# Kernel tuning notes

Measured on AMD Instinct MI355X. Metric: run time of the kernel, lower is better.

Reference implementation:

```python
import jax, jax.numpy as jnp
import numpy as np

NUM_HEADS = 12
THETA = 10000.0

def apply_rope(x, pos, theta):
    # x: [B, H, S, d_k]; pos: [S]
    d_k = x.shape[-1]
    inv_freq = theta ** (-jnp.arange(0, d_k, 2, dtype=jnp.float32) / d_k)  # [d_k/2]
    ang = pos[:, None].astype(jnp.float32) * inv_freq[None, :]             # [S, d_k/2]
    cos, sin = jnp.cos(ang), jnp.sin(ang)
    x1, x2 = x[..., ::2], x[..., 1::2]
    out_even = x1 * cos - x2 * sin
    out_odd = x1 * sin + x2 * cos
    # interleave back to [..., d_k]
    return jnp.stack([out_even, out_odd], axis=-1).reshape(x.shape)

def setup_inputs() -> dict:
    key = jax.random.key(0)
    ks = jax.random.split(key, 5)
    B, S, D = 1, 4096, 768
    x = jax.random.normal(ks[0], (B, S, D), dtype=jnp.float32)
    scale = 0.02
    Wq = jax.random.normal(ks[1], (D, D), dtype=jnp.float32) * scale
    Wk = jax.random.normal(ks[2], (D, D), dtype=jnp.float32) * scale
    Wv = jax.random.normal(ks[3], (D, D), dtype=jnp.float32) * scale
    Wo = jax.random.normal(ks[4], (D, D), dtype=jnp.float32) * scale
    return {"x": x, "Wq": Wq, "Wk": Wk, "Wv": Wv, "Wo": Wo}

def reference(x, Wq, Wk, Wv, Wo):
    B, S, D = x.shape
    H = NUM_HEADS
    d_k = D // H
    # projections (torch Linear: y = x @ W.T, no bias)
    Q = x @ Wq.T
    K = x @ Wk.T
    V = x @ Wv.T
    # [B, S, H*d_k] -> [B, H, S, d_k]
    def split_heads(t):
        return t.reshape(B, S, H, d_k).transpose(0, 2, 1, 3)
    Q, K, V = split_heads(Q), split_heads(K), split_heads(V)
    pos = jnp.arange(S)
    Q = apply_rope(Q, pos, THETA)
    K = apply_rope(K, pos, THETA)
    scores = jnp.einsum('bhnd,bhmd->bhnm', Q, K) * (d_k ** -0.5)  # [B,H,S,S]
    causal = jnp.tril(jnp.ones((S, S), dtype=bool))
    scores = jnp.where(causal, scores, -jnp.inf)
    attn = jax.nn.softmax(scores, axis=-1)
    out = jnp.einsum('bhnm,bhmd->bhnd', attn, V)  # [B,H,S,d_k]
    out = out.transpose(0, 2, 1, 3).reshape(B, S, D)
    return out @ Wo.T
```

## Files before the change

### kernel.cpp

```cpp
#include <hip/hip_runtime.h>
#include <hip/hip_bf16.h>
#include <cstdint>

typedef __bf16 bf16x8 __attribute__((ext_vector_type(8)));
typedef float f32x4 __attribute__((ext_vector_type(4)));
typedef float f32x16 __attribute__((ext_vector_type(16)));

static constexpr int S = 4096;
static constexpr int D = 768;
static constexpr int DK = 64;

__device__ __forceinline__ unsigned short f2bf(float f) {
  unsigned u = __float_as_uint(f);
  u = (u + 0x7fffu + ((u >> 16) & 1u)) >> 16;
  return (unsigned short)u;
}

__global__ __launch_bounds__(256) void cvt5_kernel(
    const float* __restrict__ x, const float* __restrict__ wq,
    const float* __restrict__ wk, const float* __restrict__ wv,
    const float* __restrict__ wo,
    unsigned short* __restrict__ xb, unsigned short* __restrict__ wqb,
    unsigned short* __restrict__ wkb, unsigned short* __restrict__ wvb,
    unsigned short* __restrict__ wob, float2* __restrict__ tab) {
  int i = blockIdx.x * blockDim.x + threadIdx.x;
  constexpr int NX4 = (S * D) / 4;
  constexpr int NW4 = (D * D) / 4;
  constexpr int NC = NX4 + 4 * NW4;
  if (i < NC) {
    const float* src;
    unsigned short* dst;
    int off;
    if (i < NX4)               { src = x;  dst = xb;  off = i; }
    else if (i < NX4 + NW4)    { src = wq; dst = wqb; off = i - NX4; }
    else if (i < NX4 + 2*NW4)  { src = wk; dst = wkb; off = i - NX4 - NW4; }
    else if (i < NX4 + 3*NW4)  { src = wv; dst = wvb; off = i - NX4 - 2*NW4; }
    else                       { src = wo; dst = wob; off = i - NX4 - 3*NW4; }
    float4 v = reinterpret_cast<const float4*>(src)[off];
    ushort4 o;
    o.x = f2bf(v.x); o.y = f2bf(v.y); o.z = f2bf(v.z); o.w = f2bf(v.w);
    reinterpret_cast<ushort4*>(dst)[off] = o;
  } else {
    int idx = i - NC;
    if (idx < S * 32) {
      int s = idx >> 5, ii = idx & 31;
      float freq = expf(-(float)(2 * ii) * (9.210340371976184f / 64.0f));
      float si, c;
      sincosf((float)s * freq, &si, &c);
      tab[idx] = make_float2(c, si);
    }
  }
}

__global__ __launch_bounds__(512) void qkv_gemm_kernel(
    const unsigned short* __restrict__ xb,
    const unsigned short* __restrict__ Wall,
    const float2* __restrict__ tab,
    unsigned short* __restrict__ Qh,
    unsigned short* __restrict__ Kf,
    unsigned short* __restrict__ Vf) {
  __shared__ alignas(16) unsigned short At[2][128 * 64];
  __shared__ alignas(16) unsigned short Bt[2][128 * 64];

  const int t = threadIdx.x;
  const int lane = t & 63;
  const int lr = lane & 15;
  const int hi = lane >> 4;
  const int wave = t >> 6;
  const int wr = wave >> 1, wc = wave & 1;
  const int row0 = blockIdx.x * 128;
  const int n0 = blockIdx.y * 128;
  const int sx = lr & 7;

  f32x4 acc[2][4] = {};

  auto stage = [&](int buf, int k0) {
#pragma unroll
    for (int j = 0; j < 2; ++j) {
      const int ci = wave * 128 + j * 64 + lane;
      const int row = ci >> 3;
      const int c16 = ci & 7;
      const int csrc = (c16 ^ (row & 7)) * 8;
      __builtin_amdgcn_global_load_lds(
          (const __attribute__((address_space(1))) void*)(
              xb + (size_t)(row0 + row) * 768 + k0 + csrc),
          (__attribute__((address_space(3))) void*)(&At[buf][row * 64 + c16 * 8]),
          16, 0, 0);
      __builtin_amdgcn_global_load_lds(
          (const __attribute__((address_space(1))) void*)(
              Wall + (size_t)(n0 + row) * 768 + k0 + csrc),
          (__attribute__((address_space(3))) void*)(&Bt[buf][row * 64 + c16 * 8]),
          16, 0, 0);
    }
  };

  stage(0, 0);
  __syncthreads();

#pragma unroll
  for (int ts = 0; ts < 12; ++ts) {
    const int cur = ts & 1;
    if (ts + 1 < 12) stage(cur ^ 1, (ts + 1) * 64);
#pragma unroll
    for (int kk = 0; kk < 2; ++kk) {
      const int csw = ((kk * 4 + hi) ^ sx) * 8;
      bf16x8 a[2], b[4];
#pragma unroll
      for (int rf = 0; rf < 2; ++rf)
        a[rf] = *reinterpret_cast<const bf16x8*>(
            &At[cur][(wr * 32 + rf * 16 + lr) * 64 + csw]);
#pragma unroll
      for (int nf = 0; nf < 4; ++nf)
        b[nf] = *reinterpret_cast<const bf16x8*>(
            &Bt[cur][(wc * 64 + nf * 16 + lr) * 64 + csw]);
#pragma unroll
      for (int rf = 0; rf < 2; ++rf)
#pragma unroll
        for (int nf = 0; nf < 4; ++nf)
          acc[rf][nf] = __builtin_amdgcn_mfma_f32_16x16x32_bf16(a[rf], b[nf], acc[rf][nf], 0, 0, 0);
    }
    __syncthreads();
  }

  const int z = n0 / 768;

  if (z < 2) {
#pragma unroll
    for (int nf = 0; nf < 4; ++nf) {
      const int c = n0 - z * 768 + wc * 64 + nf * 16 + lr;
      const int hh = c >> 6;
      const int dk = c & 63;
      const int ii = dk >> 1;
#pragma unroll
      for (int rf = 0; rf < 2; ++rf) {
        const int jrow = row0 + wr * 32 + rf * 16 + hi * 4;
#pragma unroll
        for (int j = 0; j < 4; ++j) {
          float v = acc[rf][nf][j];
          const int s = jrow + j;
          float pv = __shfl_xor(v, 1);
          float2 cs = tab[(size_t)s * 32 + ii];
          v = (dk & 1) ? (pv * cs.y + v * cs.x) : (v * cs.x - pv * cs.y);
          if (z == 0) {
            Qh[((size_t)hh * S + s) * DK + dk] = f2bf(v * 0.18033688f);
          } else {
            const size_t koff = ((size_t)hh * 128 + (s >> 5)) * 2048 +
                                (size_t)(dk >> 4) * 512 + ((dk >> 3) & 1) * 256 +
                                (s & 31) * 8 + (dk & 7);
            Kf[koff] = f2bf(v);
          }
        }
      }
    }
  } else {
#pragma unroll
    for (int nf = 0; nf < 4; ++nf) {
      const int c = n0 - 1536 + wc * 64 + nf * 16 + lr;
      const int hh = c >> 6;
      const int dv = c & 63;
#pragma unroll
      for (int rf = 0; rf < 2; ++rf) {
        const int jrow = row0 + wr * 32 + rf * 16 + hi * 4;
#pragma unroll
        for (int j = 0; j < 4; ++j) {
          const int s = jrow + j;
          const size_t voff = ((size_t)hh * 256 + (s >> 4)) * 1024 +
                              (size_t)(dv >> 5) * 512 + (dv & 31) * 16 +
                              ((s >> 3) & 1) * 8 + (s & 7);
          Vf[voff] = f2bf(acc[rf][nf][j]);
        }
      }
    }
  }
}

__global__ __launch_bounds__(256) void attn_kernel(
    const unsigned short* __restrict__ Qh,
    const unsigned short* __restrict__ Kf,
    const unsigned short* __restrict__ Vf,
    unsigned short* __restrict__ AO) {
  const int c = blockIdx.x;
  const int sslot = blockIdx.y;
  const int m3 = 3 * (c >> 1);
  const int g = sslot / 3, r = sslot - 3 * g;
  int h, qt;
  if ((c & 1) == 0) {
    if (r == 0)      { h = m3;     qt = 127 - 2 * g; }
    else if (r == 1) { h = m3 + 1; qt = 127 - 2 * g; }
    else             { h = m3;     qt = 126 - 2 * g; }
  } else {
    if (r == 0)      { h = m3 + 2; qt = 127 - 2 * g; }
    else if (r == 1) { h = m3 + 2; qt = 126 - 2 * g; }
    else             { h = m3 + 1; qt = 126 - 2 * g; }
  }

  const int wave = threadIdx.x >> 6;
  const int lane = threadIdx.x & 63;
  const int lq = lane & 31;
  const int hi2 = lane >> 5;
  const int q0w = qt * 32;
  const int qg = q0w + lq;

  const unsigned short* Qp = Qh + ((size_t)h * S + qg) * DK + hi2 * 8;
  const unsigned short* Kfp = Kf + (size_t)h * (S * DK) + hi2 * 256 + lq * 8;
  const unsigned short* Vfp = Vf + (size_t)h * (S * DK) + lq * 16 + hi2 * 8;

  bf16x8 qf[4];
#pragma unroll
  for (int ks = 0; ks < 4; ++ks)
    qf[ks] = *reinterpret_cast<const bf16x8*>(Qp + ks * 16);

  f32x16 acc0 = {}, acc1 = {};
  float lsum[4] = {0.f, 0.f, 0.f, 0.f};

  const int kvmax = ((q0w + 31) >> 6) << 6;
  const int kvfirst = 64 * wave;

  bf16x8 ka[2][4];
  if (kvfirst <= kvmax) {
    const unsigned short* K0 = Kfp + ((size_t)(kvfirst >> 5)) * 2048;
#pragma unroll
    for (int tt = 0; tt < 2; ++tt)
#pragma unroll
      for (int ks = 0; ks < 4; ++ks)
        ka[tt][ks] = *reinterpret_cast<const bf16x8*>(K0 + (size_t)tt * 2048 + ks * 512);
  }

  for (int kv0 = kvfirst; kv0 <= kvmax; kv0 += 256) {
    bf16x8 vb[2][4];
#pragma unroll
    for (int dvh = 0; dvh < 2; ++dvh)
#pragma unroll
      for (int ks = 0; ks < 4; ++ks)
        vb[dvh][ks] = *reinterpret_cast<const bf16x8*>(
            Vfp + ((size_t)(kv0 >> 4) + ks) * 1024 + dvh * 512);

    f32x16 s0 = {}, s1 = {};
#pragma unroll
    for (int ks = 0; ks < 4; ++ks) {
      s0 = __builtin_amdgcn_mfma_f32_32x32x16_bf16(ka[0][ks], qf[ks], s0, 0, 0, 0);
      s1 = __builtin_amdgcn_mfma_f32_32x32x16_bf16(ka[1][ks], qf[ks], s1, 0, 0, 0);
    }

    if ((kv0 + 256) <= kvmax) {
      const unsigned short* Kn = Kfp + ((size_t)((kv0 + 256) >> 5)) * 2048;
#pragma unroll
      for (int tt = 0; tt < 2; ++tt)
#pragma unroll
        for (int ks = 0; ks < 4; ++ks)
          ka[tt][ks] = *reinterpret_cast<const bf16x8*>(Kn + (size_t)tt * 2048 + ks * 512);
    }

    if ((kv0 + 63) > q0w) {
#pragma unroll
      for (int rr = 0; rr < 16; ++rr) {
        const int kvr = kv0 + (rr & 3) + 8 * (rr >> 2) + 4 * hi2;
        if (kvr > qg) s0[rr] = -1e30f;
        if (kvr + 32 > qg) s1[rr] = -1e30f;
      }
    }

#pragma unroll
    for (int rr = 0; rr < 16; ++rr) {
      float e0, e1;
      asm("v_exp_f32 %0, %1" : "=v"(e0) : "v"(s0[rr]));
      asm("v_exp_f32 %0, %1" : "=v"(e1) : "v"(s1[rr]));
      s0[rr] = e0;
      s1[rr] = e1;
      lsum[rr & 3] += e0 + e1;
    }

    bf16x8 pa[4];
#pragma unroll
    for (int ks = 0; ks < 4; ++ks) {
      const int a4 = 8 * (ks & 1);
      unsigned X01, X23, Y01, Y23;
      if (ks < 2) {
        asm("v_cvt_pk_bf16_f32 %0, %1, %2" : "=v"(X01) : "v"(s0[a4 + 0]), "v"(s0[a4 + 1]));
        asm("v_cvt_pk_bf16_f32 %0, %1, %2" : "=v"(X23) : "v"(s0[a4 + 2]), "v"(s0[a4 + 3]));
        asm("v_cvt_pk_bf16_f32 %0, %1, %2" : "=v"(Y01) : "v"(s0[a4 + 4]), "v"(s0[a4 + 5]));
        asm("v_cvt_pk_bf16_f32 %0, %1, %2" : "=v"(Y23) : "v"(s0[a4 + 6]), "v"(s0[a4 + 7]));
      } else {
        asm("v_cvt_pk_bf16_f32 %0, %1, %2" : "=v"(X01) : "v"(s1[a4 + 0]), "v"(s1[a4 + 1]));
        asm("v_cvt_pk_bf16_f32 %0, %1, %2" : "=v"(X23) : "v"(s1[a4 + 2]), "v"(s1[a4 + 3]));
        asm("v_cvt_pk_bf16_f32 %0, %1, %2" : "=v"(Y01) : "v"(s1[a4 + 4]), "v"(s1[a4 + 5]));
        asm("v_cvt_pk_bf16_f32 %0, %1, %2" : "=v"(Y23) : "v"(s1[a4 + 6]), "v"(s1[a4 + 7]));
      }
      asm volatile("v_permlane32_swap_b32 %0, %1" : "+v"(X01), "+v"(Y01));
      asm volatile("v_permlane32_swap_b32 %0, %1" : "+v"(X23), "+v"(Y23));
      union { unsigned u[4]; bf16x8 v; } P;
      P.u[0] = X01; P.u[1] = X23; P.u[2] = Y01; P.u[3] = Y23;
      pa[ks] = P.v;
    }

#pragma unroll
    for (int ks = 0; ks < 4; ++ks) {
      acc0 = __builtin_amdgcn_mfma_f32_32x32x16_bf16(pa[ks], vb[0][ks], acc0, 0, 0, 0);
      acc1 = __builtin_amdgcn_mfma_f32_32x32x16_bf16(pa[ks], vb[1][ks], acc1, 0, 0, 0);
    }
  }

  const float lw = (lsum[0] + lsum[1]) + (lsum[2] + lsum[3]);
  const float l_ = lw + __shfl_xor(lw, 32);

  __shared__ float llds[4][32];
  __shared__ float obuf[4][64][17];

  if (hi2 == 0) llds[wave][lq] = l_;

#pragma unroll
  for (int rr = 0; rr < 16; ++rr) obuf[wave][lane][rr] = acc0[rr];
  __syncthreads();

  const float Ltot = llds[0][lq] + llds[1][lq] + llds[2][lq] + llds[3][lq];
  const float linv = 1.0f / Ltot;

  float v0[4];
#pragma unroll
  for (int rr = 0; rr < 4; ++rr) {
    const int rq = wave * 4 + rr;
    v0[rr] = obuf[0][lane][rq] + obuf[1][lane][rq] + obuf[2][lane][rq] + obuf[3][lane][rq];
  }
  __syncthreads();

#pragma unroll
  for (int rr = 0; rr < 16; ++rr) obuf[wave][lane][rr] = acc1[rr];
  __syncthreads();

#pragma unroll
  for (int rr = 0; rr < 4; ++rr) {
    const int rq = wave * 4 + rr;
    const float v1 = obuf[0][lane][rq] + obuf[1][lane][rq] + obuf[2][lane][rq] + obuf[3][lane][rq];
    const int row = (rq & 3) + 8 * (rq >> 2) + 4 * hi2;
    const float li = __shfl(linv, row);
    const size_t s = q0w + row;
    AO[s * D + h * DK + lq]      = f2bf(v0[rr] * li);
    AO[s * D + h * DK + 32 + lq] = f2bf(v1 * li);
  }
}

__global__ __launch_bounds__(256) void oproj_kernel(
    const unsigned short* __restrict__ AO,
    const unsigned short* __restrict__ Wob,
    float* __restrict__ out) {
  __shared__ alignas(16) unsigned short At[2][128 * 64];
  __shared__ alignas(16) unsigned short Bt[2][128 * 64];

  const int t = threadIdx.x;
  const int lane = t & 63;
  const int lr = lane & 15;
  const int hi = lane >> 4;
  const int wave = t >> 6;
  const int wr = wave >> 1, wc = wave & 1;
  const int row0 = blockIdx.x * 128;
  const int n0 = blockIdx.y * 128;

  const int trow = t >> 3;
  const int tc8  = (t & 7) * 8;
  const int tsw8 = (((t & 7) ^ (trow & 7)) * 8);
  const int sx = lr & 7;

  f32x4 acc[4][4] = {};

  auto stage = [&](int buf, int k0) {
#pragma unroll
    for (int i = 0; i < 4; ++i) {
      __builtin_amdgcn_global_load_lds(
          (const __attribute__((address_space(1))) void*)(
              AO + (size_t)(row0 + trow + 32 * i) * 768 + k0 + tsw8),
          (__attribute__((address_space(3))) void*)(&At[buf][(trow + 32 * i) * 64 + tc8]),
          16, 0, 0);
      __builtin_amdgcn_global_load_lds(
          (const __attribute__((address_space(1))) void*)(
              Wob + (size_t)(n0 + trow + 32 * i) * 768 + k0 + tsw8),
          (__attribute__((address_space(3))) void*)(&Bt[buf][(trow + 32 * i) * 64 + tc8]),
          16, 0, 0);
    }
  };

  stage(0, 0);
  __syncthreads();

#pragma unroll
  for (int ts = 0; ts < 12; ++ts) {
    const int cur = ts & 1;
    if (ts + 1 < 12) stage(cur ^ 1, (ts + 1) * 64);
#pragma unroll
    for (int kk = 0; kk < 2; ++kk) {
      const int csw = ((kk * 4 + hi) ^ sx) * 8;
      bf16x8 a[4], b[4];
#pragma unroll
      for (int rf = 0; rf < 4; ++rf)
        a[rf] = *reinterpret_cast<const bf16x8*>(
            &At[cur][(wr * 64 + rf * 16 + lr) * 64 + csw]);
#pragma unroll
      for (int nf = 0; nf < 4; ++nf)
        b[nf] = *reinterpret_cast<const bf16x8*>(
            &Bt[cur][(wc * 64 + nf * 16 + lr) * 64 + csw]);
#pragma unroll
      for (int rf = 0; rf < 4; ++rf)
#pragma unroll
        for (int nf = 0; nf < 4; ++nf)
          acc[rf][nf] = __builtin_amdgcn_mfma_f32_16x16x32_bf16(a[rf], b[nf], acc[rf][nf], 0, 0, 0);
    }
    __syncthreads();
  }

#pragma unroll
  for (int rf = 0; rf < 4; ++rf) {
    const int jrow = row0 + wr * 64 + rf * 16 + hi * 4;
#pragma unroll
    for (int nf = 0; nf < 4; ++nf) {
      const int cn = n0 + wc * 64 + nf * 16 + lr;
#pragma unroll
      for (int j = 0; j < 4; ++j)
        out[(size_t)(jrow + j) * D + cn] = acc[rf][nf][j];
    }
  }
}

extern "C" void kernel_launch(void* const* d_in, const int* in_sizes, int n_in,
                              void* d_out, int out_size, void* d_ws, size_t ws_size,
                              hipStream_t stream) {
  const float* x  = (const float*)d_in[0];
  const float* Wq = (const float*)d_in[1];
  const float* Wk = (const float*)d_in[2];
  const float* Wv = (const float*)d_in[3];
  const float* Wo = (const float*)d_in[4];
  float* out = (float*)d_out;

  char* ws = (char*)d_ws;
  unsigned short* xb  = (unsigned short*)(ws + 0);
  unsigned short* Wqb = (unsigned short*)(ws + 6291456);
  unsigned short* Wkb = (unsigned short*)(ws + 7471104);
  unsigned short* Wvb = (unsigned short*)(ws + 8650752);
  unsigned short* Wob = (unsigned short*)(ws + 9830400);
  unsigned short* Qh  = (unsigned short*)(ws + 11010048);
  unsigned short* Kf  = (unsigned short*)(ws + 17301504);
  unsigned short* Vf  = (unsigned short*)(ws + 23592960);
  unsigned short* AO  = (unsigned short*)(ws + 29884416);
  float2* tab = (float2*)(ws + 29884416);

  cvt5_kernel<<<5888, 256, 0, stream>>>(x, Wq, Wk, Wv, Wo, xb, Wqb, Wkb, Wvb, Wob, tab);
  qkv_gemm_kernel<<<dim3(32, 18), 512, 0, stream>>>(xb, Wqb, tab, Qh, Kf, Vf);
  attn_kernel<<<dim3(8, 192), 256, 0, stream>>>(Qh, Kf, Vf, AO);
  oproj_kernel<<<dim3(32, 6), 256, 0, stream>>>(AO, Wob, out);
}
```

Baseline: 102.1 us.

## Halve oproj row tile to 64 and split attention row-sum accumulators

The output-projection GEMM now uses 64x128 tiles instead of 128x128, doubling the grid from 192 to 384 blocks so more of the GPU's compute units are busy. Staging loads are reorganised to fit the smaller A tile. In the attention kernel, the softmax denominator now uses 16 independent partial sums instead of 4, shortening the add dependency chains, with a tree reduction at the end. The smaller tile lowers per-block reuse of the Wo tile and adds some extra registers.

```diff
diff --git a/kernel.cpp b/kernel.cpp
--- a/kernel.cpp
+++ b/kernel.cpp
@@ -211,7 +211,9 @@
     qf[ks] = *reinterpret_cast<const bf16x8*>(Qp + ks * 16);
 
   f32x16 acc0 = {}, acc1 = {};
-  float lsum[4] = {0.f, 0.f, 0.f, 0.f};
+  float lsum[16];
+#pragma unroll
+  for (int r2 = 0; r2 < 16; ++r2) lsum[r2] = 0.f;
 
   const int kvmax = ((q0w + 31) >> 6) << 6;
   const int kvfirst = 64 * wave;
@@ -267,7 +269,7 @@
       asm("v_exp_f32 %0, %1" : "=v"(e1) : "v"(s1[rr]));
       s0[rr] = e0;
       s1[rr] = e1;
-      lsum[rr & 3] += e0 + e1;
+      lsum[rr] += e0 + e1;
     }
 
     bf16x8 pa[4];
@@ -300,8 +302,12 @@
     }
   }
 
-  const float lw = (lsum[0] + lsum[1]) + (lsum[2] + lsum[3]);
-  const float l_ = lw + __shfl_xor(lw, 32);
+#pragma unroll
+  for (int off = 8; off > 0; off >>= 1)
+#pragma unroll
+    for (int rr = 0; rr < 8; ++rr)
+      if (rr < off) lsum[rr] += lsum[rr + off];
+  const float l_ = lsum[0] + __shfl_xor(lsum[0], 32);
 
   __shared__ float llds[4][32];
   __shared__ float obuf[4][64][17];
@@ -343,7 +349,7 @@
     const unsigned short* __restrict__ AO,
     const unsigned short* __restrict__ Wob,
     float* __restrict__ out) {
-  __shared__ alignas(16) unsigned short At[2][128 * 64];
+  __shared__ alignas(16) unsigned short At[2][64 * 64];
   __shared__ alignas(16) unsigned short Bt[2][128 * 64];
 
   const int t = threadIdx.x;
@@ -352,28 +358,35 @@
   const int hi = lane >> 4;
   const int wave = t >> 6;
   const int wr = wave >> 1, wc = wave & 1;
-  const int row0 = blockIdx.x * 128;
+  const int row0 = blockIdx.x * 64;
   const int n0 = blockIdx.y * 128;
-
-  const int trow = t >> 3;
-  const int tc8  = (t & 7) * 8;
-  const int tsw8 = (((t & 7) ^ (trow & 7)) * 8);
   const int sx = lr & 7;
 
-  f32x4 acc[4][4] = {};
+  f32x4 acc[2][4] = {};
 
   auto stage = [&](int buf, int k0) {
 #pragma unroll
-    for (int i = 0; i < 4; ++i) {
+    for (int p = 0; p < 2; ++p) {
+      const int ci = p * 256 + t;
+      const int row = ci >> 3;
+      const int c16 = ci & 7;
+      const int csrc = (c16 ^ (row & 7)) * 8;
       __builtin_amdgcn_global_load_lds(
           (const __attribute__((address_space(1))) void*)(
-              AO + (size_t)(row0 + trow + 32 * i) * 768 + k0 + tsw8),
-          (__attribute__((address_space(3))) void*)(&At[buf][(trow + 32 * i) * 64 + tc8]),
+              AO + (size_t)(row0 + row) * 768 + k0 + csrc),
+          (__attribute__((address_space(3))) void*)(&At[buf][row * 64 + c16 * 8]),
           16, 0, 0);
+    }
+#pragma unroll
+    for (int p = 0; p < 4; ++p) {
+      const int ci = p * 256 + t;
+      const int row = ci >> 3;
+      const int c16 = ci & 7;
+      const int csrc = (c16 ^ (row & 7)) * 8;
       __builtin_amdgcn_global_load_lds(
           (const __attribute__((address_space(1))) void*)(
-              Wob + (size_t)(n0 + trow + 32 * i) * 768 + k0 + tsw8),
-          (__attribute__((address_space(3))) void*)(&Bt[buf][(trow + 32 * i) * 64 + tc8]),
+              Wob + (size_t)(n0 + row) * 768 + k0 + csrc),
+          (__attribute__((address_space(3))) void*)(&Bt[buf][row * 64 + c16 * 8]),
           16, 0, 0);
     }
   };
@@ -388,17 +401,17 @@
 #pragma unroll
     for (int kk = 0; kk < 2; ++kk) {
       const int csw = ((kk * 4 + hi) ^ sx) * 8;
-      bf16x8 a[4], b[4];
-#pragma unroll
-      for (int rf = 0; rf < 4; ++rf)
+      bf16x8 a[2], b[4];
+#pragma unroll
+      for (int rf = 0; rf < 2; ++rf)
         a[rf] = *reinterpret_cast<const bf16x8*>(
-            &At[cur][(wr * 64 + rf * 16 + lr) * 64 + csw]);
+            &At[cur][(wr * 32 + rf * 16 + lr) * 64 + csw]);
 #pragma unroll
       for (int nf = 0; nf < 4; ++nf)
         b[nf] = *reinterpret_cast<const bf16x8*>(
             &Bt[cur][(wc * 64 + nf * 16 + lr) * 64 + csw]);
 #pragma unroll
-      for (int rf = 0; rf < 4; ++rf)
+      for (int rf = 0; rf < 2; ++rf)
 #pragma unroll
         for (int nf = 0; nf < 4; ++nf)
           acc[rf][nf] = __builtin_amdgcn_mfma_f32_16x16x32_bf16(a[rf], b[nf], acc[rf][nf], 0, 0, 0);
@@ -407,8 +420,8 @@
   }
 
 #pragma unroll
-  for (int rf = 0; rf < 4; ++rf) {
-    const int jrow = row0 + wr * 64 + rf * 16 + hi * 4;
+  for (int rf = 0; rf < 2; ++rf) {
+    const int jrow = row0 + wr * 32 + rf * 16 + hi * 4;
 #pragma unroll
     for (int nf = 0; nf < 4; ++nf) {
       const int cn = n0 + wc * 64 + nf * 16 + lr;
@@ -444,5 +457,5 @@
   cvt5_kernel<<<5888, 256, 0, stream>>>(x, Wq, Wk, Wv, Wo, xb, Wqb, Wkb, Wvb, Wob, tab);
   qkv_gemm_kernel<<<dim3(32, 18), 512, 0, stream>>>(xb, Wqb, tab, Qh, Kf, Vf);
   attn_kernel<<<dim3(8, 192), 256, 0, stream>>>(Qh, Kf, Vf, AO);
-  oproj_kernel<<<dim3(32, 6), 256, 0, stream>>>(AO, Wob, out);
-}
+  oproj_kernel<<<dim3(64, 6), 256, 0, stream>>>(AO, Wob, out);
+}
```

New measurement: 98.43 us (median of 2 runs). 1.04x faster.
